# Optimization experiments

Hardware: AMD Instinct MI355X
Metric: run time of the kernel (lower is better)

## Reference

```python
import jax, jax.numpy as jnp
import numpy as np

B, N = 1, 768
C_S, C_P = 384, 128
K = 32            # relpos_k
NBIN = 2 * K + 1  # 65
EPS = 1e-10


def setup_inputs() -> dict:
    key = jax.random.key(0)
    ks = jax.random.split(key, 8)
    s = jax.random.normal(ks[0], (B, N, C_S), jnp.float32)
    trans = jax.random.normal(ks[1], (B, N, 3), jnp.float32)
    p_mask = jnp.ones((B, N, N), jnp.float32)
    # Linear params (torch default: U(-1/sqrt(fan_in), 1/sqrt(fan_in)))
    def lin(k, out_f, in_f):
        k1, k2 = jax.random.split(k)
        bound = 1.0 / np.sqrt(in_f)
        W = jax.random.uniform(k1, (out_f, in_f), jnp.float32, -bound, bound)
        b = jax.random.uniform(k2, (out_f,), jnp.float32, -bound, bound)
        return W, b
    W_i, b_i = lin(ks[2], C_P, C_S)
    W_j, b_j = lin(ks[3], C_P, C_S)
    W_rel, b_rel = lin(ks[4], C_P, NBIN)
    W_t, b_t = lin(ks[5], C_P, 1)
    return {"s": s, "trans": trans, "p_mask": p_mask,
            "W_i": W_i, "b_i": b_i, "W_j": W_j, "b_j": b_j,
            "W_rel": W_rel, "b_rel": b_rel, "W_t": W_t, "b_t": b_t}


def reference(s, trans, p_mask, W_i, b_i, W_j, b_j, W_rel, b_rel, W_t, b_t):
    # p_i + p_j broadcast sum: [B,N,1,c_p] + [B,1,N,c_p]
    p_i = jnp.einsum('bnc,pc->bnp', s, W_i) + b_i   # [B,N,c_p]
    p_j = jnp.einsum('bnc,pc->bnp', s, W_j) + b_j
    p = p_i[:, :, None, :] + p_j[:, None, :, :]      # [B,N,N,c_p]

    # relpos: r[:, :, None] - r[:, None, :] with r = arange(N) (same every batch).
    # argmin_|d - v| over v = [-K..K] with integer d has a unique minimizer == clip(d,-K,K),
    # and one_hot(b) @ W_rel.T == W_rel.T[b]  (direct gather, same math).
    r = jnp.arange(N)
    bins = jnp.clip(r[:, None] - r[None, :], -K, K) + K  # [N,N] in [0, NBIN)
    rel = jnp.take(W_rel.T, bins, axis=0) + b_rel        # [N,N,c_p]
    p = p + rel[None]

    # template v1: pairwise distance of trans, then Linear(1 -> c_p)
    diff = trans[:, :, None, :] - trans[:, None, :, :]   # [B,N,N,3]
    dist = jnp.sqrt(EPS + jnp.sum(diff * diff, axis=-1)) # [B,N,N]
    p = p + dist[..., None] * W_t[:, 0] + b_t            # Linear(1->c_p)

    p = p * p_mask[..., None]
    return p
```

## Files before the change

kernel.cpp:

```cpp
#include <hip/hip_runtime.h>
#include <math.h>

#define N 768
#define CS 384
#define CP 128
#define NBIN 65
#define MT 64

typedef float f4 __attribute__((ext_vector_type(4)));
typedef float f2 __attribute__((ext_vector_type(2)));

__global__ __launch_bounds__(256) void prep_kernel(
    const float* __restrict__ s,
    const float* __restrict__ Wi, const float* __restrict__ bi,
    const float* __restrict__ Wj, const float* __restrict__ bj,
    const float* __restrict__ Wrel, const float* __restrict__ brel,
    const float* __restrict__ bt,
    float* __restrict__ pI, float* __restrict__ pJ, float* __restrict__ relT) {
  const int tid = threadIdx.x;

  if (blockIdx.x >= N / 4) {
    const int bb = (blockIdx.x - N / 4) * 2 + (tid >> 7);
    const int p = tid & 127;
    if (bb < NBIN)
      relT[bb * CP + p] = Wrel[p * NBIN + bb] + brel[p] + bt[p];
    return;
  }

  __shared__ float s_sh[4 * CS];
  const int n0 = blockIdx.x * 4;
  for (int i = tid; i < 4 * CS / 4; i += 256)
    reinterpret_cast<f4*>(s_sh)[i] = reinterpret_cast<const f4*>(s + n0 * CS)[i];
  __syncthreads();

  const int which = tid >> 7;
  const int p = tid & 127;
  const float* W = which ? Wj : Wi;
  const float b = which ? bj[p] : bi[p];
  const f4* W4 = reinterpret_cast<const f4*>(W + p * CS);
  const f4* S4 = reinterpret_cast<const f4*>(s_sh);

  float acc0 = b, acc1 = b, acc2 = b, acc3 = b;
  for (int c4 = 0; c4 < CS / 4; ++c4) {
    const f4 w = W4[c4];
    const f4 s0 = S4[0 * (CS / 4) + c4];
    const f4 s1 = S4[1 * (CS / 4) + c4];
    const f4 s2 = S4[2 * (CS / 4) + c4];
    const f4 s3 = S4[3 * (CS / 4) + c4];
    acc0 += s0.x * w.x + s0.y * w.y + s0.z * w.z + s0.w * w.w;
    acc1 += s1.x * w.x + s1.y * w.y + s1.z * w.z + s1.w * w.w;
    acc2 += s2.x * w.x + s2.y * w.y + s2.z * w.z + s2.w * w.w;
    acc3 += s3.x * w.x + s3.y * w.y + s3.z * w.z + s3.w * w.w;
  }
  float* outp = which ? pJ : pI;
  outp[(n0 + 0) * CP + p] = acc0;
  outp[(n0 + 1) * CP + p] = acc1;
  outp[(n0 + 2) * CP + p] = acc2;
  outp[(n0 + 3) * CP + p] = acc3;
}

__global__ __launch_bounds__(256) void pair_kernel(
    const float* __restrict__ pI, const float* __restrict__ pJ,
    const float* __restrict__ relT, const float* __restrict__ Wt,
    const float* __restrict__ trans, const float* __restrict__ mask,
    float* __restrict__ out) {
  __shared__ f2 dm_sh[MT];

  const int n = blockIdx.y;
  const int m0 = blockIdx.x * MT;
  const int tid = threadIdx.x;

  if (tid < MT) {
    const int m = m0 + tid;
    const float dx = trans[n * 3 + 0] - trans[m * 3 + 0];
    const float dy = trans[n * 3 + 1] - trans[m * 3 + 1];
    const float dz = trans[n * 3 + 2] - trans[m * 3 + 2];
    f2 dm;
    dm.x = sqrtf(1e-10f + dx * dx + dy * dy + dz * dz);
    dm.y = mask[n * N + m];
    dm_sh[tid] = dm;
  }
  __syncthreads();

  const int v = tid & 31;
  const int slot = tid >> 5;

  const f4 pi4 = reinterpret_cast<const f4*>(pI)[n * (CP / 4) + v];
  const f4 wt4 = reinterpret_cast<const f4*>(Wt)[v];
  const f4* __restrict__ pJ4 = reinterpret_cast<const f4*>(pJ);
  const f4* __restrict__ rel4 = reinterpret_cast<const f4*>(relT);
  f4* __restrict__ out4 = reinterpret_cast<f4*>(out) + ((size_t)n * N + m0) * (CP / 4);

#pragma unroll
  for (int k = 0; k < MT / 8; ++k) {
    const int mi = k * 8 + slot;
    const int m = m0 + mi;
    int d = n - m;
    d = d < -32 ? -32 : (d > 32 ? 32 : d);

    const f4 pj4 = pJ4[m * (CP / 4) + v];
    const f4 rl = rel4[(d + 32) * (CP / 4) + v];
    const f2 dm = dm_sh[mi];

    f4 o;
    o.x = (pi4.x + pj4.x + rl.x + dm.x * wt4.x) * dm.y;
    o.y = (pi4.y + pj4.y + rl.y + dm.x * wt4.y) * dm.y;
    o.z = (pi4.z + pj4.z + rl.z + dm.x * wt4.z) * dm.y;
    o.w = (pi4.w + pj4.w + rl.w + dm.x * wt4.w) * dm.y;

    out4[mi * (CP / 4) + v] = o;
  }
}

extern "C" void kernel_launch(void* const* d_in, const int* in_sizes, int n_in,
                              void* d_out, int out_size, void* d_ws, size_t ws_size,
                              hipStream_t stream) {
  const float* s      = (const float*)d_in[0];
  const float* trans  = (const float*)d_in[1];
  const float* p_mask = (const float*)d_in[2];
  const float* Wi     = (const float*)d_in[3];
  const float* bi     = (const float*)d_in[4];
  const float* Wj     = (const float*)d_in[5];
  const float* bj     = (const float*)d_in[6];
  const float* Wrel   = (const float*)d_in[7];
  const float* brel   = (const float*)d_in[8];
  const float* Wt     = (const float*)d_in[9];
  const float* bt     = (const float*)d_in[10];
  float* out = (float*)d_out;

  float* ws   = (float*)d_ws;
  float* pI   = ws;
  float* pJ   = ws + N * CP;
  float* relT = ws + 2 * N * CP;

  prep_kernel<<<N / 4 + (NBIN + 1) / 2, 256, 0, stream>>>(
      s, Wi, bi, Wj, bj, Wrel, brel, bt, pI, pJ, relT);
  pair_kernel<<<dim3(N / MT, N), 256, 0, stream>>>(
      pI, pJ, relT, Wt, trans, p_mask, out);
}
```

Measured before the change: 73.43 us.

## Precompute distance/mask pairs in prep kernel and use grid-stride flat pair kernel

Moves the pairwise distance and mask computation into extra blocks of the prep kernel, which write an f2 array to workspace. The pair kernel becomes a flat grid-stride loop over all output float4s on a fixed 2048-block grid and reads these precomputed values. This removes the per-block shared-memory stage and barrier, at the cost of writing and re-reading an extra N*N*8-byte buffer and doing per-element integer division in the hot loop.

```diff
diff --git a/kernel.cpp b/kernel.cpp
--- a/kernel.cpp
+++ b/kernel.cpp
@@ -5,10 +5,15 @@
 #define CS 384
 #define CP 128
 #define NBIN 65
-#define MT 64
 
 typedef float f4 __attribute__((ext_vector_type(4)));
 typedef float f2 __attribute__((ext_vector_type(2)));
+
+#define NM (N * N)
+#define TOTAL_F4 (NM * (CP / 4))
+#define PROJ_BLOCKS (N / 4)
+#define REL_BLOCKS ((NBIN + 1) / 2)
+#define DM_BLOCKS (NM / 256)
 
 __global__ __launch_bounds__(256) void prep_kernel(
     const float* __restrict__ s,
@@ -16,11 +21,27 @@
     const float* __restrict__ Wj, const float* __restrict__ bj,
     const float* __restrict__ Wrel, const float* __restrict__ brel,
     const float* __restrict__ bt,
-    float* __restrict__ pI, float* __restrict__ pJ, float* __restrict__ relT) {
+    const float* __restrict__ trans, const float* __restrict__ mask,
+    float* __restrict__ pI, float* __restrict__ pJ, float* __restrict__ relT,
+    f2* __restrict__ dm2) {
   const int tid = threadIdx.x;
 
-  if (blockIdx.x >= N / 4) {
-    const int bb = (blockIdx.x - N / 4) * 2 + (tid >> 7);
+  if (blockIdx.x >= PROJ_BLOCKS + REL_BLOCKS) {
+    const int e = (blockIdx.x - (PROJ_BLOCKS + REL_BLOCKS)) * 256 + tid;
+    const unsigned nn = (unsigned)e / N;
+    const unsigned mm = (unsigned)e - nn * N;
+    const float dx = trans[nn * 3 + 0] - trans[mm * 3 + 0];
+    const float dy = trans[nn * 3 + 1] - trans[mm * 3 + 1];
+    const float dz = trans[nn * 3 + 2] - trans[mm * 3 + 2];
+    f2 dm;
+    dm.x = sqrtf(1e-10f + dx * dx + dy * dy + dz * dz);
+    dm.y = mask[e];
+    dm2[e] = dm;
+    return;
+  }
+
+  if (blockIdx.x >= PROJ_BLOCKS) {
+    const int bb = (blockIdx.x - PROJ_BLOCKS) * 2 + (tid >> 7);
     const int p = tid & 127;
     if (bb < NBIN)
       relT[bb * CP + p] = Wrel[p * NBIN + bb] + brel[p] + bt[p];
@@ -62,53 +83,31 @@
 __global__ __launch_bounds__(256) void pair_kernel(
     const float* __restrict__ pI, const float* __restrict__ pJ,
     const float* __restrict__ relT, const float* __restrict__ Wt,
-    const float* __restrict__ trans, const float* __restrict__ mask,
-    float* __restrict__ out) {
-  __shared__ f2 dm_sh[MT];
-
-  const int n = blockIdx.y;
-  const int m0 = blockIdx.x * MT;
-  const int tid = threadIdx.x;
-
-  if (tid < MT) {
-    const int m = m0 + tid;
-    const float dx = trans[n * 3 + 0] - trans[m * 3 + 0];
-    const float dy = trans[n * 3 + 1] - trans[m * 3 + 1];
-    const float dz = trans[n * 3 + 2] - trans[m * 3 + 2];
-    f2 dm;
-    dm.x = sqrtf(1e-10f + dx * dx + dy * dy + dz * dz);
-    dm.y = mask[n * N + m];
-    dm_sh[tid] = dm;
-  }
-  __syncthreads();
-
-  const int v = tid & 31;
-  const int slot = tid >> 5;
-
-  const f4 pi4 = reinterpret_cast<const f4*>(pI)[n * (CP / 4) + v];
-  const f4 wt4 = reinterpret_cast<const f4*>(Wt)[v];
+    const f2* __restrict__ dm2, float* __restrict__ out) {
+  const f4* __restrict__ pI4 = reinterpret_cast<const f4*>(pI);
   const f4* __restrict__ pJ4 = reinterpret_cast<const f4*>(pJ);
   const f4* __restrict__ rel4 = reinterpret_cast<const f4*>(relT);
-  f4* __restrict__ out4 = reinterpret_cast<f4*>(out) + ((size_t)n * N + m0) * (CP / 4);
+  f4* __restrict__ out4 = reinterpret_cast<f4*>(out);
 
-#pragma unroll
-  for (int k = 0; k < MT / 8; ++k) {
-    const int mi = k * 8 + slot;
-    const int m = m0 + mi;
-    int d = n - m;
+  const int stride = gridDim.x * 256;
+
+  for (int idx = blockIdx.x * 256 + threadIdx.x; idx < TOTAL_F4; idx += stride) {
+    const unsigned v = (unsigned)idx & 31u;
+    const unsigned nm = (unsigned)idx >> 5;
+    const unsigned n = nm / N;
+    const unsigned m = nm - n * N;
+
+    int d = (int)n - (int)m;
     d = d < -32 ? -32 : (d > 32 ? 32 : d);
 
+    const f4 pi4 = pI4[n * (CP / 4) + v];
     const f4 pj4 = pJ4[m * (CP / 4) + v];
-    const f4 rl = rel4[(d + 32) * (CP / 4) + v];
-    const f2 dm = dm_sh[mi];
+    const f4 rl = rel4[(unsigned)(d + 32) * (CP / 4) + v];
+    const f4 wt4 = reinterpret_cast<const f4*>(Wt)[v];
+    const f2 dm = dm2[nm];
 
-    f4 o;
-    o.x = (pi4.x + pj4.x + rl.x + dm.x * wt4.x) * dm.y;
-    o.y = (pi4.y + pj4.y + rl.y + dm.x * wt4.y) * dm.y;
-    o.z = (pi4.z + pj4.z + rl.z + dm.x * wt4.z) * dm.y;
-    o.w = (pi4.w + pj4.w + rl.w + dm.x * wt4.w) * dm.y;
-
-    out4[mi * (CP / 4) + v] = o;
+    const f4 o = (pi4 + pj4 + rl + dm.x * wt4) * dm.y;
+    out4[idx] = o;
   }
 }
 
@@ -132,9 +131,9 @@
   float* pI   = ws;
   float* pJ   = ws + N * CP;
   float* relT = ws + 2 * N * CP;
+  f2*   dm2   = reinterpret_cast<f2*>(ws + 2 * N * CP + NBIN * CP);
 
-  prep_kernel<<<N / 4 + (NBIN + 1) / 2, 256, 0, stream>>>(
-      s, Wi, bi, Wj, bj, Wrel, brel, bt, pI, pJ, relT);
-  pair_kernel<<<dim3(N / MT, N), 256, 0, stream>>>(
-      pI, pJ, relT, Wt, trans, p_mask, out);
+  prep_kernel<<<PROJ_BLOCKS + REL_BLOCKS + DM_BLOCKS, 256, 0, stream>>>(
+      s, Wi, bi, Wj, bj, Wrel, brel, bt, trans, p_mask, pI, pJ, relT, dm2);
+  pair_kernel<<<2048, 256, 0, stream>>>(pI, pJ, relT, Wt, dm2, out);
 }
```

New measurement: 78.40 us. +6.8%, slower.
